# Optimization experiments

Hardware: AMD Instinct MI355X
Metric: run time of the kernel (lower is better)

The kernel has to match this reference:

```python
import jax, jax.numpy as jnp
import numpy as np

BN_EPS = 1e-6
SOFTMAX_EPS = 1e-8
D = 64      # fingerprint_dim
BD = 12     # bond_dim
N_ATOM = 10000
N_EDGE = 40000


def _bn(x, gamma, beta, mean, var):
    # BatchNorm1d in inference mode (running stats)
    return (x - mean) / jnp.sqrt(var + BN_EPS) * gamma + beta


def setup_inputs() -> dict:
    key = jax.random.key(0)
    ks = jax.random.split(key, 16)
    inp = {
        "atom": jax.random.normal(ks[0], (N_ATOM, D), dtype=jnp.float32),
        "bond_index": jax.random.randint(ks[1], (N_EDGE, 2), 0, N_ATOM, dtype=jnp.int64),
        "bond": jax.random.normal(ks[2], (N_EDGE, BD), dtype=jnp.float32),
        # encoder: Linear(bond_dim, D*D) + BatchNorm1d(D*D)
        "enc_W": jax.random.normal(ks[3], (D * D, BD), dtype=jnp.float32) * (1.0 / np.sqrt(BD)),
        "enc_b": jnp.zeros((D * D,), dtype=jnp.float32),
        "enc_gamma": jnp.ones((D * D,), dtype=jnp.float32),
        "enc_beta": jnp.zeros((D * D,), dtype=jnp.float32),
        "enc_mean": jnp.zeros((D * D,), dtype=jnp.float32),
        "enc_var": jnp.ones((D * D,), dtype=jnp.float32),
        # align: Linear(2*D, 1)
        "align_W": jax.random.normal(ks[4], (1, 2 * D), dtype=jnp.float32) * (1.0 / np.sqrt(2 * D)),
        "align_b": jnp.zeros((1,), dtype=jnp.float32),
        # attend: Linear(D, D) + BatchNorm1d(D), no activation
        "att_W": jax.random.normal(ks[5], (D, D), dtype=jnp.float32) * (1.0 / np.sqrt(D)),
        "att_b": jnp.zeros((D,), dtype=jnp.float32),
        "att_gamma": jnp.ones((D,), dtype=jnp.float32),
        "att_beta": jnp.zeros((D,), dtype=jnp.float32),
        "att_mean": jnp.zeros((D,), dtype=jnp.float32),
        "att_var": jnp.ones((D,), dtype=jnp.float32),
        # GRUCell(D, D)
        "gru_W_ih": jax.random.normal(ks[6], (3 * D, D), dtype=jnp.float32) * (1.0 / np.sqrt(D)),
        "gru_W_hh": jax.random.normal(ks[7], (3 * D, D), dtype=jnp.float32) * (1.0 / np.sqrt(D)),
        "gru_b_ih": jnp.zeros((3 * D,), dtype=jnp.float32),
        "gru_b_hh": jnp.zeros((3 * D,), dtype=jnp.float32),
    }
    return inp


def reference(atom, bond_index, bond,
              enc_W, enc_b, enc_gamma, enc_beta, enc_mean, enc_var,
              align_W, align_b,
              att_W, att_b, att_gamma, att_beta, att_mean, att_var,
              gru_W_ih, gru_W_hh, gru_b_ih, gru_b_hh):
    num_atom, d = atom.shape
    tgt = bond_index[:, 0]  # target atom of each edge
    nbr = bond_index[:, 1]  # neighbor atom of each edge

    # encoder: relu(BN(linear(bond))) -> per-edge [d, d] bond matrix
    enc = jax.nn.relu(_bn(bond @ enc_W.T + enc_b, enc_gamma, enc_beta, enc_mean, enc_var))
    enc = enc.reshape(-1, d, d)  # [E, d, d]

    # gather neighbor atoms, per-edge matvec through bond matrix
    neighbor = jnp.einsum('ed,edf->ef', atom[nbr], enc)  # [E, d]

    # attention logits (dropout is identity in eval)
    feat = jnp.concatenate([atom[tgt], neighbor], axis=-1)  # [E, 2d]
    score = jax.nn.leaky_relu(feat @ align_W.T + align_b, negative_slope=0.01)  # [E, 1]

    # segment softmax over target atoms
    mx = jax.ops.segment_max(score, tgt, num_segments=num_atom)  # [N, 1]
    ex = jnp.exp(score - mx[tgt])
    denom = jax.ops.segment_sum(ex, tgt, num_segments=num_atom)[tgt] + SOFTMAX_EPS
    attn = ex / denom  # [E, 1]

    # attend: BN(linear(neighbor)) (no activation), weighted scatter-add
    attd = _bn(neighbor @ att_W.T + att_b, att_gamma, att_beta, att_mean, att_var)
    context = jax.ops.segment_sum(attn * attd, tgt, num_segments=num_atom)  # [N, d]
    context = jax.nn.elu(context)

    # GRUCell(context, atom)
    gi = context @ gru_W_ih.T + gru_b_ih  # [N, 3d]
    gh = atom @ gru_W_hh.T + gru_b_hh     # [N, 3d]
    i_r, i_z, i_n = jnp.split(gi, 3, axis=-1)
    h_r, h_z, h_n = jnp.split(gh, 3, axis=-1)
    r = jax.nn.sigmoid(i_r + h_r)
    z = jax.nn.sigmoid(i_z + h_z)
    n = jnp.tanh(i_n + r * h_n)
    return (1.0 - z) * n + z * atom
```

## Files before the change

kernel.cpp:

```cpp
#include <hip/hip_runtime.h>
#include <math.h>

#define NA 10000
#define NE 40000

typedef float f4 __attribute__((ext_vector_type(4)));
typedef float f16v __attribute__((ext_vector_type(16)));
typedef int   i4 __attribute__((ext_vector_type(4)));
typedef __bf16 bf16x8 __attribute__((ext_vector_type(8)));

union U8 { unsigned short us[8]; bf16x8 v; };

static __device__ __forceinline__ unsigned short bf_rne(float x){
  unsigned u = __float_as_uint(x);
  unsigned r = (u + 0x7fffu + ((u>>16)&1u)) >> 16;
  return (unsigned short)r;
}
static __device__ __forceinline__ float bf_to_f(unsigned short h){
  return __uint_as_float(((unsigned)h)<<16);
}

__global__ __launch_bounds__(256) void k_pre(
  const float* __restrict__ encW, const float* __restrict__ encB,
  const float* __restrict__ eg, const float* __restrict__ ebt,
  const float* __restrict__ e_mn, const float* __restrict__ e_vr,
  const float* __restrict__ attW, const float* __restrict__ attB,
  const float* __restrict__ agm, const float* __restrict__ abt,
  const float* __restrict__ amn, const float* __restrict__ avr,
  const float* __restrict__ wih, const float* __restrict__ whh,
  const int* __restrict__ bidx, const float* __restrict__ atom,
  const float* __restrict__ alW,
  unsigned short* __restrict__ Bh, unsigned short* __restrict__ Bl,
  unsigned short* __restrict__ aBh, unsigned short* __restrict__ aBl,
  float* __restrict__ attBf, float* __restrict__ wT,
  float* __restrict__ p, int* __restrict__ cnt)
{
  int tid = threadIdx.x;
  int gid = blockIdx.x*256 + tid;
  int gstride = gridDim.x*256;
  for (int i=gid; i<65536; i+=gstride){
    int j = i&7, ll = (i>>3)&63, t = i>>9;
    int d = t>>1, ft = t&1;
    int k = ((ll>>5)<<3)+j;
    int n = d*64 + ft*32 + (ll&31);
    float s = eg[n]*rsqrtf(e_vr[n]+1e-6f);
    unsigned short vh=0, vl=0;
    if (k<12){
      float wv = encW[n*12+k]*s;
      unsigned short hi = bf_rne(wv);
      vh = hi; vl = bf_rne(wv - bf_to_f(hi));
    } else if (k==12){
      float b = (encB[n]-e_mn[n])*s + ebt[n];
      unsigned short hi = bf_rne(b);
      vh = hi; vl = bf_rne(b - bf_to_f(hi));
    }
    Bh[i] = vh; Bl[i] = vl;
  }
  for (int i=gid; i<4096; i+=gstride){
    int j=i&7, l=(i>>3)&63, t=i>>9;
    int kk=t>>1, nt=t&1;
    int k = kk*16 + ((l>>5)<<3) + j;
    int n = nt*32 + (l&31);
    float s = agm[n]*rsqrtf(avr[n]+1e-6f);
    float wv = attW[n*64+k]*s;
    unsigned short hi = bf_rne(wv);
    aBh[i]=hi; aBl[i]=bf_rne(wv - bf_to_f(hi));
  }
  for (int f=gid; f<64; f+=gstride){
    float s = agm[f]*rsqrtf(avr[f]+1e-6f);
    attBf[f] = (attB[f]-amn[f])*s + abt[f];
  }
  for (int i=gid; i<24576; i+=gstride){
    int j=i&3, f=(i>>2)&63, idx2=i>>8;
    int g=idx2>>4, kg=idx2&15, k=kg*4+j;
    wT[i] = (g<3)? wih[(g*64+f)*64+k] : whh[((g-3)*64+f)*64+k];
  }
  {
    int wid = gid>>6;
    int l = tid&63;
    float wl = alW[l];
    for (int a=wid; a<NA; a+=(gstride>>6)){
      float v = wl*atom[(size_t)a*64+l];
      v += __shfl_xor(v,1);  v += __shfl_xor(v,2);
      v += __shfl_xor(v,4);  v += __shfl_xor(v,8);
      v += __shfl_xor(v,16); v += __shfl_xor(v,32);
      if (l==0) p[a]=v;
    }
  }
  for (int e=gid; e<NE; e+=gstride) atomicAdd(&cnt[bidx[e*2]],1);
}

__global__ __launch_bounds__(256) void k_scan(const int* __restrict__ cnt,
                                              int* __restrict__ rowstart,
                                              int* __restrict__ wofs)
{
  __shared__ int sPart[256];
  int t = threadIdx.x;
  int base = t*40;
  i4 buf[10];
  int sum = 0;
  if (base < NA){
    const i4* cp = (const i4*)(cnt + base);
    #pragma unroll
    for (int i=0;i<10;i++) buf[i] = cp[i];
    #pragma unroll
    for (int i=0;i<10;i++) sum += buf[i].x+buf[i].y+buf[i].z+buf[i].w;
  }
  sPart[t]=sum;
  __syncthreads();
  for (int off=1; off<256; off<<=1){
    int v = (t>=off)? sPart[t-off] : 0;
    __syncthreads();
    sPart[t]+=v;
    __syncthreads();
  }
  int run = sPart[t]-sum;
  if (base < NA){
    #pragma unroll
    for (int i=0;i<10;i++){
      i4 b=buf[i], o;
      o.x=run; run+=b.x; o.y=run; run+=b.y;
      o.z=run; run+=b.z; o.w=run; run+=b.w;
      ((i4*)(rowstart+base))[i]=o;
      ((i4*)(wofs+base))[i]=o;
    }
  }
  if (t==0) rowstart[NA]=NE;
}

__global__ __launch_bounds__(256) void k_scatter(const int* __restrict__ bidx,
                                                 int* __restrict__ wofs,
                                                 int* __restrict__ elist)
{
  int e = blockIdx.x*256 + threadIdx.x;
  if (e < NE){
    int tg = bidx[e*2];
    int pos = atomicAdd(&wofs[tg],1);
    elist[pos]=e;
  }
}

__global__ __launch_bounds__(256) void k_edge(
  const float* __restrict__ atom, const int* __restrict__ bidx, const float* __restrict__ bond,
  const unsigned short* __restrict__ Bh, const unsigned short* __restrict__ Bl,
  const unsigned short* __restrict__ aBh, const unsigned short* __restrict__ aBl,
  const float* __restrict__ alW,
  const int* __restrict__ elist, float* __restrict__ zC, float* __restrict__ qv)
{
  __shared__ float sA[4352];
  __shared__ float sP[4096];
  __shared__ int   sEl[64];
  __shared__ int   sNbr[64];

  int tid = threadIdx.x;
  int l = tid & 63;
  int w = tid >> 6;
  int g = l >> 5;
  int em = l & 31;
  int E0 = blockIdx.x * 64;

  if (tid < 64){
    int e = elist[E0+tid];
    sEl[tid] = e;
    sNbr[tid] = bidx[e*2+1];
  }
  __syncthreads();
  for (int i=tid; i<4096; i+=256){
    int le=i>>6, d=i&63;
    sA[d*68+le] = atom[(size_t)sNbr[le]*64 + d];
  }

  U8 A1[2], A2[2];
  #pragma unroll
  for (int t=0;t<2;t++){
    const f4* bp = (const f4*)(bond + (size_t)sEl[t*32+em]*12);
    f4 b0=bp[0], b1v=bp[1], b2v=bp[2];
    float bv[12] = {b0.x,b0.y,b0.z,b0.w,b1v.x,b1v.y,b1v.z,b1v.w,b2v.x,b2v.y,b2v.z,b2v.w};
    unsigned short hi[12], lo2[12];
    #pragma unroll
    for (int j=0;j<12;j++){ hi[j]=bf_rne(bv[j]); lo2[j]=bf_rne(bv[j]-bf_to_f(hi[j])); }
    #pragma unroll
    for (int j=0;j<8;j++){
      int k = g*8+j;
      A1[t].us[j] = (k<12)? hi[k] : (k==12? (unsigned short)0x3F80 : (unsigned short)0);
      A2[t].us[j] = (k<12)? lo2[k] : (unsigned short)0;
    }
  }
  __syncthreads();

  int ft = w & 1;
  int dbase = (w >> 1) * 32;

  f4 nacc[2][4];
  #pragma unroll
  for (int t=0;t<2;t++)
    #pragma unroll
    for (int q=0;q<4;q++) nacc[t][q] = (f4){0.f,0.f,0.f,0.f};
  f16v cz;
  #pragma unroll
  for (int r=0;r<16;r++) cz[r] = 0.f;

  U8 cbh, cbl;
  cbh.v = *(const bf16x8*)(Bh + ((size_t)((dbase*2+ft)*64 + l))*8);
  cbl.v = *(const bf16x8*)(Bl + ((size_t)((dbase*2+ft)*64 + l))*8);

  #pragma unroll 2
  for (int dd=0; dd<32; dd++){
    int d = dbase + dd;
    int dn = (dd<31)? d+1 : d;
    U8 nbh, nbl;
    nbh.v = *(const bf16x8*)(Bh + ((size_t)((dn*2+ft)*64 + l))*8);
    nbl.v = *(const bf16x8*)(Bl + ((size_t)((dn*2+ft)*64 + l))*8);

    f4 ldA[2][4];
    #pragma unroll
    for (int t=0;t<2;t++)
      #pragma unroll
      for (int q=0;q<4;q++) ldA[t][q] = *(const f4*)&sA[d*68 + t*32 + 8*q + 4*g];

    #pragma unroll
    for (int t=0;t<2;t++){
      f16v c;
      c = __builtin_amdgcn_mfma_f32_32x32x16_bf16(A1[t].v, cbh.v, cz, 0,0,0);
      c = __builtin_amdgcn_mfma_f32_32x32x16_bf16(A2[t].v, cbh.v, c, 0,0,0);
      c = __builtin_amdgcn_mfma_f32_32x32x16_bf16(A1[t].v, cbl.v, c, 0,0,0);
      #pragma unroll
      for (int r=0;r<16;r++){
        float ev = fmaxf(c[r], 0.f);
        nacc[t][r>>2][r&3] = fmaf(ldA[t][r>>2][r&3], ev, nacc[t][r>>2][r&3]);
      }
    }
    cbh = nbh; cbl = nbl;
  }

  __syncthreads();
  if (w >= 2){
    #pragma unroll
    for (int t=0;t<2;t++)
      #pragma unroll
      for (int r=0;r<16;r++)
        sP[(w-2)*2048 + t*1024 + r*64 + l] = nacc[t][r>>2][r&3];
  }
  __syncthreads();
  if (w < 2){
    #pragma unroll
    for (int t=0;t<2;t++)
      #pragma unroll
      for (int r=0;r<16;r++){
        float v = nacc[t][r>>2][r&3] + sP[w*2048 + t*1024 + r*64 + l];
        int m = t*32 + (r&3) + ((r>>2)<<3) + (g<<2);
        sA[m*68 + (w<<5) + em] = v;
      }
  }
  __syncthreads();

  {
    float alwn = alW[64+l];
    #pragma unroll 4
    for (int i=0;i<16;i++){
      int le = w*16 + i;
      float qq = sA[le*68 + l] * alwn;
      qq += __shfl_xor(qq,1);  qq += __shfl_xor(qq,2);
      qq += __shfl_xor(qq,4);  qq += __shfl_xor(qq,8);
      qq += __shfl_xor(qq,16); qq += __shfl_xor(qq,32);
      if (l==0) qv[E0+le] = qq;
    }
  }
  {
    f16v c;
    #pragma unroll
    for (int r=0;r<16;r++) c[r] = 0.f;
    int mt2 = w>>1, nt = w&1;
    #pragma unroll
    for (int kk=0; kk<4; kk++){
      const float* src = &sA[(mt2*32+em)*68 + kk*16 + g*8];
      f4 x0 = *(const f4*)src;
      f4 x1 = *(const f4*)(src+4);
      U8 Ah, Al;
      #pragma unroll
      for (int j=0;j<4;j++){
        unsigned short h0 = bf_rne(x0[j]);
        Ah.us[j] = h0; Al.us[j] = bf_rne(x0[j]-bf_to_f(h0));
        unsigned short h1 = bf_rne(x1[j]);
        Ah.us[4+j] = h1; Al.us[4+j] = bf_rne(x1[j]-bf_to_f(h1));
      }
      U8 bh, bl;
      bh.v = *(const bf16x8*)(aBh + ((size_t)((kk*2+nt)*64 + l))*8);
      bl.v = *(const bf16x8*)(aBl + ((size_t)((kk*2+nt)*64 + l))*8);
      c = __builtin_amdgcn_mfma_f32_32x32x16_bf16(Ah.v, bh.v, c, 0,0,0);
      c = __builtin_amdgcn_mfma_f32_32x32x16_bf16(Al.v, bh.v, c, 0,0,0);
      c = __builtin_amdgcn_mfma_f32_32x32x16_bf16(Ah.v, bl.v, c, 0,0,0);
    }
    #pragma unroll
    for (int r=0;r<16;r++){
      int row = (r&3) + ((r>>2)<<3) + ((l>>5)<<2);
      zC[(size_t)(E0 + mt2*32 + row)*64 + nt*32 + (l&31)] = c[r];
    }
  }
}

__global__ __launch_bounds__(256, 4) void k_gru(
  const float* __restrict__ atom, const float* __restrict__ zC,
  const int* __restrict__ rowstart, const float* __restrict__ p,
  const float* __restrict__ qv, const float* __restrict__ alB,
  const float* __restrict__ attBf, const float* __restrict__ wT,
  const float* __restrict__ bih, const float* __restrict__ bhh,
  float* __restrict__ out)
{
  __shared__ float sc[4][2][64];
  __shared__ float shh[4][2][64];
  int tid = threadIdx.x;
  int l = tid & 63;
  int w = tid >> 6;
  int base = blockIdx.x*8 + w*2;
  float bias = attBf[l];
  float ab = alB[0];

  #pragma unroll
  for (int aa=0; aa<2; aa++){
    int a = base + aa;
    float cf=0.f, hf=0.f;
    if (a < NA){
      hf = atom[(size_t)a*64 + l];
      int d0 = rowstart[a];
      int deg = rowstart[a+1] - d0;
      if (deg > 0){
        float pa = p[a] + ab;
        float mx = -1e30f;
        #pragma unroll 1
        for (int i=0;i<deg;i++){
          float s = pa + qv[d0+i];
          s = (s>0.f)? s : 0.01f*s;
          mx = fmaxf(mx, s);
        }
        float dn = 0.f, y = 0.f;
        #pragma unroll 1
        for (int i=0;i<deg;i++){
          float s = pa + qv[d0+i];
          s = (s>0.f)? s : 0.01f*s;
          float ex = __expf(s - mx);
          dn += ex;
          y = fmaf(ex, zC[(size_t)(d0+i)*64 + l], y);
        }
        cf = (y + dn*bias)/(dn + 1e-8f);
        cf = (cf>0.f)? cf : expm1f(cf);
      }
    }
    sc[w][aa][l] = cf; shh[w][aa][l] = hf;
  }
  __syncthreads();

  float acc[6][2];
  #pragma unroll
  for (int gg=0;gg<6;gg++){ acc[gg][0]=0.f; acc[gg][1]=0.f; }

  #pragma unroll 2
  for (int kg=0; kg<16; kg++){
    f4 wv[6];
    #pragma unroll
    for (int gg=0;gg<6;gg++) wv[gg] = *(const f4*)&wT[(size_t)((gg*16+kg)*64 + l)*4];
    #pragma unroll
    for (int aa=0;aa<2;aa++){
      f4 cv = *(const f4*)&sc[w][aa][kg*4];
      f4 hv = *(const f4*)&shh[w][aa][kg*4];
      #pragma unroll
      for (int j=0;j<4;j++){
        acc[0][aa] = fmaf(cv[j], wv[0][j], acc[0][aa]);
        acc[1][aa] = fmaf(cv[j], wv[1][j], acc[1][aa]);
        acc[2][aa] = fmaf(cv[j], wv[2][j], acc[2][aa]);
        acc[3][aa] = fmaf(hv[j], wv[3][j], acc[3][aa]);
        acc[4][aa] = fmaf(hv[j], wv[4][j], acc[4][aa]);
        acc[5][aa] = fmaf(hv[j], wv[5][j], acc[5][aa]);
      }
    }
  }

  float b0 = bih[l], b1 = bih[64+l], b2 = bih[128+l];
  float h0 = bhh[l], h1 = bhh[64+l], h2 = bhh[128+l];
  #pragma unroll
  for (int aa=0;aa<2;aa++){
    int a = base + aa;
    if (a < NA){
      float hf = shh[w][aa][l];
      float r = 1.f/(1.f + expf(-(acc[0][aa] + b0 + acc[3][aa] + h0)));
      float z = 1.f/(1.f + expf(-(acc[1][aa] + b1 + acc[4][aa] + h1)));
      float n = tanhf(acc[2][aa] + b2 + r*(acc[5][aa] + h2));
      out[(size_t)a*64 + l] = (1.f - z)*n + z*hf;
    }
  }
}

extern "C" void kernel_launch(void* const* d_in, const int* in_sizes, int n_in,
                              void* d_out, int out_size, void* d_ws, size_t ws_size,
                              hipStream_t stream) {
  const float* atom = (const float*)d_in[0];
  const int*   bidx = (const int*)  d_in[1];
  const float* bond = (const float*)d_in[2];
  const float* encW = (const float*)d_in[3];
  const float* encB = (const float*)d_in[4];
  const float* eg   = (const float*)d_in[5];
  const float* ebt  = (const float*)d_in[6];
  const float* e_mn = (const float*)d_in[7];
  const float* e_vr = (const float*)d_in[8];
  const float* alW  = (const float*)d_in[9];
  const float* alB  = (const float*)d_in[10];
  const float* atW  = (const float*)d_in[11];
  const float* atB  = (const float*)d_in[12];
  const float* agm  = (const float*)d_in[13];
  const float* abt  = (const float*)d_in[14];
  const float* amn  = (const float*)d_in[15];
  const float* avr  = (const float*)d_in[16];
  const float* wih  = (const float*)d_in[17];
  const float* whh  = (const float*)d_in[18];
  const float* bih  = (const float*)d_in[19];
  const float* bhh  = (const float*)d_in[20];

  float* ws = (float*)d_ws;
  unsigned short* Bh  = (unsigned short*)(ws + 0);
  unsigned short* Bl  = (unsigned short*)(ws + 32768);
  unsigned short* aBh = (unsigned short*)(ws + 65536);
  unsigned short* aBl = (unsigned short*)(ws + 67584);
  float* attBf   = ws + 69632;
  float* wT      = ws + 69696;
  float* p       = ws + 94272;
  int*   cnt     = (int*)(ws + 104288);
  int*   rowstart= (int*)(ws + 114304);
  int*   wofs    = (int*)(ws + 124320);
  int*   elist   = (int*)(ws + 134336);
  float* qv      = ws + 174336;
  float* zCb     = ws + 214336;
  float* outp    = (float*)d_out;

  hipMemsetAsync(cnt, 0, NA*sizeof(int), stream);
  k_pre<<<512, 256, 0, stream>>>(encW,encB,eg,ebt,e_mn,e_vr,
                                 atW,atB,agm,abt,amn,avr,
                                 wih,whh,bidx,atom,alW,
                                 Bh,Bl,aBh,aBl,attBf,wT,p,cnt);
  k_scan<<<1, 256, 0, stream>>>(cnt, rowstart, wofs);
  k_scatter<<<(NE+255)/256, 256, 0, stream>>>(bidx, wofs, elist);
  k_edge<<<625, 256, 0, stream>>>(atom, bidx, bond, Bh, Bl, aBh, aBl, alW,
                                  elist, zCb, qv);
  k_gru<<<1250, 256, 0, stream>>>(atom, zCb, rowstart, p, qv, alB,
                                  attBf, wT, bih, bhh, outp);
}
```

Before: 183.1 us.

## Deepen B prefetch, use packed FMA accumulation, and single-pass online softmax

In the edge kernel, the B-fragment prefetch now runs two iterations ahead instead of one, the loop is unrolled 4x, and the ReLU-weighted accumulation uses inline v_pk_fma_f32 on float2 pairs to halve the FMA instruction count. In the atom kernel, the two-pass segment softmax becomes a single-pass online softmax with rescaling, so qv is read once per edge. The aim is to hide global-load latency and cut VALU work, at the cost of more live registers and a data-dependent branch in the softmax loop.

New measurement: 180.5 us. No clear change (-1.4%).

```diff
diff --git a/kernel.cpp b/kernel.cpp
--- a/kernel.cpp
+++ b/kernel.cpp
@@ -4,12 +4,15 @@
 #define NA 10000
 #define NE 40000
 
+typedef float f2 __attribute__((ext_vector_type(2)));
 typedef float f4 __attribute__((ext_vector_type(4)));
 typedef float f16v __attribute__((ext_vector_type(16)));
 typedef int   i4 __attribute__((ext_vector_type(4)));
 typedef __bf16 bf16x8 __attribute__((ext_vector_type(8)));
 
 union U8 { unsigned short us[8]; bf16x8 v; };
+union UF4 { f4 v; f2 h[2]; };
+union UC16 { f16v v; f2 h[8]; };
 
 static __device__ __forceinline__ unsigned short bf_rne(float x){
   unsigned u = __float_as_uint(x);
@@ -191,63 +194,68 @@
   int ft = w & 1;
   int dbase = (w >> 1) * 32;
 
-  f4 nacc[2][4];
+  f2 nacc[2][8];
   #pragma unroll
   for (int t=0;t<2;t++)
     #pragma unroll
-    for (int q=0;q<4;q++) nacc[t][q] = (f4){0.f,0.f,0.f,0.f};
+    for (int i=0;i<8;i++) nacc[t][i] = (f2){0.f,0.f};
   f16v cz;
   #pragma unroll
   for (int r=0;r<16;r++) cz[r] = 0.f;
 
-  U8 cbh, cbl;
-  cbh.v = *(const bf16x8*)(Bh + ((size_t)((dbase*2+ft)*64 + l))*8);
-  cbl.v = *(const bf16x8*)(Bl + ((size_t)((dbase*2+ft)*64 + l))*8);
-
-  #pragma unroll 2
+  const bf16x8* pH = (const bf16x8*)Bh + ((size_t)(dbase*2+ft)*64 + l);
+  const bf16x8* pL = (const bf16x8*)Bl + ((size_t)(dbase*2+ft)*64 + l);
+  U8 b0h, b0l, b1h, b1l;
+  b0h.v = pH[0];   b0l.v = pL[0];
+  b1h.v = pH[128]; b1l.v = pL[128];
+
+  #pragma unroll 4
   for (int dd=0; dd<32; dd++){
     int d = dbase + dd;
-    int dn = (dd<31)? d+1 : d;
-    U8 nbh, nbl;
-    nbh.v = *(const bf16x8*)(Bh + ((size_t)((dn*2+ft)*64 + l))*8);
-    nbl.v = *(const bf16x8*)(Bl + ((size_t)((dn*2+ft)*64 + l))*8);
-
-    f4 ldA[2][4];
+    U8 b2h, b2l;
+    b2h.v = pH[(dd+2)*128];
+    b2l.v = pL[(dd+2)*128];
+
+    UF4 ldA[2][4];
     #pragma unroll
     for (int t=0;t<2;t++)
       #pragma unroll
-      for (int q=0;q<4;q++) ldA[t][q] = *(const f4*)&sA[d*68 + t*32 + 8*q + 4*g];
+      for (int q=0;q<4;q++) ldA[t][q].v = *(const f4*)&sA[d*68 + t*32 + 8*q + 4*g];
 
     #pragma unroll
     for (int t=0;t<2;t++){
-      f16v c;
-      c = __builtin_amdgcn_mfma_f32_32x32x16_bf16(A1[t].v, cbh.v, cz, 0,0,0);
-      c = __builtin_amdgcn_mfma_f32_32x32x16_bf16(A2[t].v, cbh.v, c, 0,0,0);
-      c = __builtin_amdgcn_mfma_f32_32x32x16_bf16(A1[t].v, cbl.v, c, 0,0,0);
+      UC16 c;
+      c.v = __builtin_amdgcn_mfma_f32_32x32x16_bf16(A1[t].v, b0h.v, cz, 0,0,0);
+      c.v = __builtin_amdgcn_mfma_f32_32x32x16_bf16(A2[t].v, b0h.v, c.v, 0,0,0);
+      c.v = __builtin_amdgcn_mfma_f32_32x32x16_bf16(A1[t].v, b0l.v, c.v, 0,0,0);
+      #pragma unroll
+      for (int i=0;i<8;i++){
+        f2 ev;
+        ev[0] = fmaxf(c.h[i][0], 0.f);
+        ev[1] = fmaxf(c.h[i][1], 0.f);
+        asm("v_pk_fma_f32 %0, %1, %2, %0"
+            : "+v"(nacc[t][i])
+            : "v"(ldA[t][i>>1].h[i&1]), "v"(ev));
+      }
+    }
+    b0h = b1h; b0l = b1l; b1h = b2h; b1l = b2l;
+  }
+
+  __syncthreads();
+  if (w >= 2){
+    #pragma unroll
+    for (int t=0;t<2;t++)
+      #pragma unroll
+      for (int r=0;r<16;r++)
+        sP[(w-2)*2048 + t*1024 + r*64 + l] = nacc[t][r>>1][r&1];
+  }
+  __syncthreads();
+  if (w < 2){
+    #pragma unroll
+    for (int t=0;t<2;t++)
       #pragma unroll
       for (int r=0;r<16;r++){
-        float ev = fmaxf(c[r], 0.f);
-        nacc[t][r>>2][r&3] = fmaf(ldA[t][r>>2][r&3], ev, nacc[t][r>>2][r&3]);
-      }
-    }
-    cbh = nbh; cbl = nbl;
-  }
-
-  __syncthreads();
-  if (w >= 2){
-    #pragma unroll
-    for (int t=0;t<2;t++)
-      #pragma unroll
-      for (int r=0;r<16;r++)
-        sP[(w-2)*2048 + t*1024 + r*64 + l] = nacc[t][r>>2][r&3];
-  }
-  __syncthreads();
-  if (w < 2){
-    #pragma unroll
-    for (int t=0;t<2;t++)
-      #pragma unroll
-      for (int r=0;r<16;r++){
-        float v = nacc[t][r>>2][r&3] + sP[w*2048 + t*1024 + r*64 + l];
+        float v = nacc[t][r>>1][r&1] + sP[w*2048 + t*1024 + r*64 + l];
         int m = t*32 + (r&3) + ((r>>2)<<3) + (g<<2);
         sA[m*68 + (w<<5) + em] = v;
       }
@@ -326,21 +334,18 @@
       int deg = rowstart[a+1] - d0;
       if (deg > 0){
         float pa = p[a] + ab;
-        float mx = -1e30f;
-        #pragma unroll 1
+        float mx = -3e38f, dn = 0.f, y = 0.f;
         for (int i=0;i<deg;i++){
           float s = pa + qv[d0+i];
           s = (s>0.f)? s : 0.01f*s;
-          mx = fmaxf(mx, s);
-        }
-        float dn = 0.f, y = 0.f;
-        #pragma unroll 1
-        for (int i=0;i<deg;i++){
-          float s = pa + qv[d0+i];
-          s = (s>0.f)? s : 0.01f*s;
+          float zc = zC[(size_t)(d0+i)*64 + l];
+          if (s > mx){
+            float al = __expf(mx - s);
+            dn *= al; y *= al; mx = s;
+          }
           float ex = __expf(s - mx);
           dn += ex;
-          y = fmaf(ex, zC[(size_t)(d0+i)*64 + l], y);
+          y = fmaf(ex, zc, y);
         }
         cf = (y + dn*bias)/(dn + 1e-8f);
         cf = (cf>0.f)? cf : expm1f(cf);
```
